# Kernel tuning notes

Hardware: AMD Instinct MI355X
Metric: run time of the kernel (lower is better)

The kernel has to match this reference:

```python
import jax, jax.numpy as jnp
import numpy as np

CHANNELS = 1024
HEADS = 16


def setup_inputs() -> dict:
    key = jax.random.key(0)
    k1, k2, k3, k4 = jax.random.split(key, 4)
    x = jax.random.normal(k1, (32, 8192, CHANNELS), dtype=jnp.float32)
    query = jax.random.normal(k2, (HEADS, CHANNELS), dtype=jnp.float32)
    proj_w = jax.random.normal(k3, (CHANNELS, CHANNELS), dtype=jnp.float32) * (CHANNELS ** -0.5)
    proj_b = jax.random.normal(k4, (CHANNELS,), dtype=jnp.float32) * 0.01
    return {"x": x, "query": query, "proj_w": proj_w, "proj_b": proj_b}


def reference(x, query, proj_w, proj_b):
    scale = x.shape[-1] ** -0.5
    # scores: [b, t, h]
    scores = jnp.einsum('btc,hc->bth', x, query) * scale
    attn = jax.nn.softmax(scores, axis=1)  # softmax over sequence dim
    pooled = jnp.einsum('bth,btc->bhc', attn, x)  # [b, h, c]
    pooled = pooled.mean(axis=1)  # head-mean -> [b, c]
    return pooled @ proj_w.T + proj_b
```

## Files before the change

### kernel.cpp

```cpp
#include <hip/hip_runtime.h>

#define CHANNELS 1024
#define HEADS 16
#define BATCH 32
#define SEQ 8192
#define NCHUNK 16
#define TCHUNK (SEQ / NCHUNK)

#define ACC_FLOATS (BATCH * NCHUNK * HEADS * CHANNELS)
#define L_OFF      ACC_FLOATS
#define L_FLOATS   (BATCH * NCHUNK * HEADS)
#define PM_OFF     (ACC_FLOATS + L_FLOATS)

__device__ __forceinline__ float dot4(float4 a, float4 b) {
    float s = a.x * b.x;
    s = fmaf(a.y, b.y, s);
    s = fmaf(a.z, b.z, s);
    s = fmaf(a.w, b.w, s);
    return s;
}

__global__ __launch_bounds__(256, 2)
void k1_scores_acc(const float* __restrict__ x, const float* __restrict__ q,
                   float* __restrict__ ws) {
    const int tid  = threadIdx.x;
    const int lane = tid & 63;
    const int w    = tid >> 6;
    const int b    = blockIdx.x >> 4;
    const int ck   = blockIdx.x & 15;

    const int cbase = 4 * lane;

    float4 qr[4][4];
#pragma unroll
    for (int h = 0; h < 4; ++h) {
        const float* qp = q + (4 * w + h) * CHANNELS + cbase;
#pragma unroll
        for (int k = 0; k < 4; ++k)
            qr[h][k] = *(const float4*)(qp + 256 * k);
    }

    float4 acc[4][4];
    float  l[4];
#pragma unroll
    for (int h = 0; h < 4; ++h) {
        l[h] = 0.0f;
#pragma unroll
        for (int k = 0; k < 4; ++k)
            acc[h][k] = make_float4(0.f, 0.f, 0.f, 0.f);
    }

    const float* xrow = x + (size_t)(b * SEQ + ck * TCHUNK) * CHANNELS;
    const float scale = 0.03125f;

    float4 xc[4];
#pragma unroll
    for (int k = 0; k < 4; ++k)
        xc[k] = *(const float4*)(xrow + cbase + 256 * k);

    for (int r = 0; r < TCHUNK; ++r) {
        const int rn = (r + 1 < TCHUNK) ? (r + 1) : r;
        const float* nx = xrow + rn * CHANNELS + cbase;
        float4 xn[4];
#pragma unroll
        for (int k = 0; k < 4; ++k)
            xn[k] = *(const float4*)(nx + 256 * k);

        float p[4];
#pragma unroll
        for (int h = 0; h < 4; ++h) {
            float s = dot4(xc[0], qr[h][0]);
            s += dot4(xc[1], qr[h][1]);
            s += dot4(xc[2], qr[h][2]);
            s += dot4(xc[3], qr[h][3]);
            p[h] = s;
        }

#pragma unroll
        for (int h = 0; h < 4; ++h) {
            p[h] += __shfl_xor(p[h], 32, 64);
            p[h] += __shfl_xor(p[h], 16, 64);
            p[h] += __shfl_xor(p[h],  8, 64);
            p[h] += __shfl_xor(p[h],  4, 64);
            p[h] += __shfl_xor(p[h],  2, 64);
            p[h] += __shfl_xor(p[h],  1, 64);
        }

#pragma unroll
        for (int h = 0; h < 4; ++h) {
            const float e = __expf(p[h] * scale);
            l[h] += e;
#pragma unroll
            for (int k = 0; k < 4; ++k) {
                acc[h][k].x = fmaf(e, xc[k].x, acc[h][k].x);
                acc[h][k].y = fmaf(e, xc[k].y, acc[h][k].y);
                acc[h][k].z = fmaf(e, xc[k].z, acc[h][k].z);
                acc[h][k].w = fmaf(e, xc[k].w, acc[h][k].w);
            }
        }

#pragma unroll
        for (int k = 0; k < 4; ++k) xc[k] = xn[k];
    }

    const int blk = b * NCHUNK + ck;
    float* accp = ws + ((size_t)(blk * HEADS + 4 * w)) * CHANNELS;
#pragma unroll
    for (int h = 0; h < 4; ++h) {
#pragma unroll
        for (int k = 0; k < 4; ++k)
            *(float4*)(accp + h * CHANNELS + cbase + 256 * k) = acc[h][k];
    }
    if (lane == 0) {
        *(float4*)(ws + L_OFF + blk * HEADS + 4 * w) =
            make_float4(l[0], l[1], l[2], l[3]);
    }
}

__global__ __launch_bounds__(256)
void k2_merge(float* __restrict__ ws) {
    const int b = blockIdx.x;
    const int tid = threadIdx.x;

    __shared__ float lt[HEADS][NCHUNK + 1];
    __shared__ float linv[HEADS];

    {
        const int h = tid & 15, ck = tid >> 4;
        lt[h][ck] = ws[L_OFF + (b * NCHUNK + ck) * HEADS + h];
    }
    __syncthreads();
    if (tid < HEADS) {
        float s = 0.f;
#pragma unroll
        for (int ck = 0; ck < NCHUNK; ++ck) s += lt[tid][ck];
        linv[tid] = 1.0f / (16.0f * s);
    }
    __syncthreads();

    const int c = 4 * tid;
    float4 pm = make_float4(0.f, 0.f, 0.f, 0.f);
#pragma unroll 1
    for (int h = 0; h < HEADS; ++h) {
        float4 hs = make_float4(0.f, 0.f, 0.f, 0.f);
        for (int ck = 0; ck < NCHUNK; ++ck) {
            const float4 v =
                *(const float4*)(ws + ((size_t)((b * NCHUNK + ck) * HEADS + h)) * CHANNELS + c);
            hs.x += v.x; hs.y += v.y; hs.z += v.z; hs.w += v.w;
        }
        const float wi = linv[h];
        pm.x = fmaf(wi, hs.x, pm.x);
        pm.y = fmaf(wi, hs.y, pm.y);
        pm.z = fmaf(wi, hs.z, pm.z);
        pm.w = fmaf(wi, hs.w, pm.w);
    }
    *(float4*)(ws + PM_OFF + b * CHANNELS + c) = pm;
}

__global__ __launch_bounds__(64)
void k3_proj(const float* __restrict__ W, const float* __restrict__ bias,
             const float* __restrict__ ws, float* __restrict__ out) {
    const int lane = threadIdx.x;
    const int b  = blockIdx.x >> 4;
    const int jt = blockIdx.x & 15;
    const int cbase = 4 * lane;

    const float* pm = ws + PM_OFF + b * CHANNELS;
    float4 pmr[4];
#pragma unroll
    for (int k = 0; k < 4; ++k)
        pmr[k] = *(const float4*)(pm + cbase + 256 * k);

    for (int jj = 0; jj < 64; ++jj) {
        const int j = jt * 64 + jj;
        const float* wr = W + (size_t)j * CHANNELS + cbase;
        float s = 0.f;
#pragma unroll
        for (int k = 0; k < 4; ++k)
            s += dot4(*(const float4*)(wr + 256 * k), pmr[k]);

        s += __shfl_xor(s, 32, 64);
        s += __shfl_xor(s, 16, 64);
        s += __shfl_xor(s,  8, 64);
        s += __shfl_xor(s,  4, 64);
        s += __shfl_xor(s,  2, 64);
        s += __shfl_xor(s,  1, 64);

        if (lane == 0) out[b * CHANNELS + j] = s + bias[j];
    }
}

extern "C" void kernel_launch(void* const* d_in, const int* in_sizes, int n_in,
                              void* d_out, int out_size, void* d_ws, size_t ws_size,
                              hipStream_t stream) {
    const float* x    = (const float*)d_in[0];
    const float* q    = (const float*)d_in[1];
    const float* W    = (const float*)d_in[2];
    const float* bias = (const float*)d_in[3];
    float* out = (float*)d_out;
    float* ws  = (float*)d_ws;

    k1_scores_acc<<<dim3(BATCH * NCHUNK), dim3(256), 0, stream>>>(x, q, ws);
    k2_merge<<<dim3(BATCH), dim3(256), 0, stream>>>(ws);
    k3_proj<<<dim3(BATCH * 16), dim3(64), 0, stream>>>(W, bias, ws, out);
}
```

Baseline: 1.545 ms.

## Transpose-reduce head scores, unroll row loop by two, widen merge and proj grids

The score reduction in k1 now exchanges partial sums across lane halves so that 4 heads share one butterfly: three select-and-shuffle steps plus four full shuffles instead of 24. Each lane then computes one exp2 and redistributes the values with shuffles, and the output head index is remapped to match. The row loop is unrolled by two with ping-pong prefetch buffers. k2 is split across 8 column tiles per batch with a shared-memory reduction over chunks, and k3 uses twice as many blocks, to raise parallelism in the small tail kernels. The main aim is to cut shuffle and ALU overhead in the dominant k1 loop, which may already be bound by memory bandwidth.

Result: faster. 1.503 ms (-2.7%).

```diff
diff --git a/kernel.cpp b/kernel.cpp
--- a/kernel.cpp
+++ b/kernel.cpp
@@ -19,6 +19,8 @@
     s = fmaf(a.w, b.w, s);
     return s;
 }
+
+#define SCALE2 0.045084690834743236f
 
 __global__ __launch_bounds__(256, 2)
 void k1_scores_acc(const float* __restrict__ x, const float* __restrict__ q,
@@ -29,7 +31,10 @@
     const int b    = blockIdx.x >> 4;
     const int ck   = blockIdx.x & 15;
 
-    const int cbase = 4 * lane;
+    const int  cbase = 4 * lane;
+    const bool hi32  = (lane & 32) != 0;
+    const bool hi16  = (lane & 16) != 0;
+    const int  g     = (lane >> 4) & 3;
 
     float4 qr[4][4];
 #pragma unroll
@@ -43,73 +48,93 @@
     float4 acc[4][4];
     float  l[4];
 #pragma unroll
-    for (int h = 0; h < 4; ++h) {
-        l[h] = 0.0f;
-#pragma unroll
-        for (int k = 0; k < 4; ++k)
-            acc[h][k] = make_float4(0.f, 0.f, 0.f, 0.f);
-    }
-
-    const float* xrow = x + (size_t)(b * SEQ + ck * TCHUNK) * CHANNELS;
-    const float scale = 0.03125f;
-
-    float4 xc[4];
+    for (int j = 0; j < 4; ++j) {
+        l[j] = 0.0f;
+#pragma unroll
+        for (int k = 0; k < 4; ++k)
+            acc[j][k] = make_float4(0.f, 0.f, 0.f, 0.f);
+    }
+
+    const float* xrow = x + (size_t)(b * SEQ + ck * TCHUNK) * CHANNELS + cbase;
+
+#define PROCESS_ROW(XC)                                                        \
+    {                                                                          \
+        float p0 = dot4(XC[0], qr[0][0]); p0 += dot4(XC[1], qr[0][1]);         \
+        p0 += dot4(XC[2], qr[0][2]);      p0 += dot4(XC[3], qr[0][3]);         \
+        float p1 = dot4(XC[0], qr[1][0]); p1 += dot4(XC[1], qr[1][1]);         \
+        p1 += dot4(XC[2], qr[1][2]);      p1 += dot4(XC[3], qr[1][3]);         \
+        float p2 = dot4(XC[0], qr[2][0]); p2 += dot4(XC[1], qr[2][1]);         \
+        p2 += dot4(XC[2], qr[2][2]);      p2 += dot4(XC[3], qr[2][3]);         \
+        float p3 = dot4(XC[0], qr[3][0]); p3 += dot4(XC[1], qr[3][1]);         \
+        p3 += dot4(XC[2], qr[3][2]);      p3 += dot4(XC[3], qr[3][3]);         \
+                                       \
+        float tA = hi32 ? p0 : p2;                                             \
+        float rA = __shfl_xor(tA, 32, 64);                                     \
+        float A  = (hi32 ? p2 : p0) + rA;                    \
+        float tB = hi32 ? p1 : p3;                                             \
+        float rB = __shfl_xor(tB, 32, 64);                                     \
+        float B  = (hi32 ? p3 : p1) + rB;                    \
+                                       \
+        float tC = hi16 ? A : B;                                               \
+        float rC = __shfl_xor(tC, 16, 64);                                     \
+        float S  = (hi16 ? B : A) + rC;                            \
+                                          \
+        S += __shfl_xor(S, 8, 64);                                             \
+        S += __shfl_xor(S, 4, 64);                                             \
+        S += __shfl_xor(S, 2, 64);                                             \
+        S += __shfl_xor(S, 1, 64);                                             \
+                    \
+        const float E0 = exp2f(S * SCALE2);                      \
+        const float E1 = __shfl_xor(E0, 16, 64);                 \
+        const float E2 = __shfl_xor(E0, 32, 64);                 \
+        const float E3 = __shfl_xor(E1, 32, 64);                 \
+        const float e[4] = {E0, E1, E2, E3};                                   \
+        l[0] += E0; l[1] += E1; l[2] += E2; l[3] += E3;                        \
+        _Pragma("unroll")                                                      \
+        for (int j = 0; j < 4; ++j) {                                          \
+            const float ev = e[j];                                             \
+            _Pragma("unroll")                                                  \
+            for (int k = 0; k < 4; ++k) {                                      \
+                acc[j][k].x = fmaf(ev, XC[k].x, acc[j][k].x);                  \
+                acc[j][k].y = fmaf(ev, XC[k].y, acc[j][k].y);                  \
+                acc[j][k].z = fmaf(ev, XC[k].z, acc[j][k].z);                  \
+                acc[j][k].w = fmaf(ev, XC[k].w, acc[j][k].w);                  \
+            }                                                                  \
+        }                                                                      \
+    }
+
+    float4 xa[4], xb[4];
 #pragma unroll
     for (int k = 0; k < 4; ++k)
-        xc[k] = *(const float4*)(xrow + cbase + 256 * k);
-
-    for (int r = 0; r < TCHUNK; ++r) {
-        const int rn = (r + 1 < TCHUNK) ? (r + 1) : r;
-        const float* nx = xrow + rn * CHANNELS + cbase;
-        float4 xn[4];
-#pragma unroll
-        for (int k = 0; k < 4; ++k)
-            xn[k] = *(const float4*)(nx + 256 * k);
-
-        float p[4];
-#pragma unroll
-        for (int h = 0; h < 4; ++h) {
-            float s = dot4(xc[0], qr[h][0]);
-            s += dot4(xc[1], qr[h][1]);
-            s += dot4(xc[2], qr[h][2]);
-            s += dot4(xc[3], qr[h][3]);
-            p[h] = s;
-        }
-
-#pragma unroll
-        for (int h = 0; h < 4; ++h) {
-            p[h] += __shfl_xor(p[h], 32, 64);
-            p[h] += __shfl_xor(p[h], 16, 64);
-            p[h] += __shfl_xor(p[h],  8, 64);
-            p[h] += __shfl_xor(p[h],  4, 64);
-            p[h] += __shfl_xor(p[h],  2, 64);
-            p[h] += __shfl_xor(p[h],  1, 64);
-        }
-
-#pragma unroll
-        for (int h = 0; h < 4; ++h) {
-            const float e = __expf(p[h] * scale);
-            l[h] += e;
-#pragma unroll
-            for (int k = 0; k < 4; ++k) {
-                acc[h][k].x = fmaf(e, xc[k].x, acc[h][k].x);
-                acc[h][k].y = fmaf(e, xc[k].y, acc[h][k].y);
-                acc[h][k].z = fmaf(e, xc[k].z, acc[h][k].z);
-                acc[h][k].w = fmaf(e, xc[k].w, acc[h][k].w);
-            }
-        }
-
-#pragma unroll
-        for (int k = 0; k < 4; ++k) xc[k] = xn[k];
-    }
+        xa[k] = *(const float4*)(xrow + 256 * k);
+
+    for (int r = 0; r < TCHUNK; r += 2) {
+        {
+            const float* nx = xrow + (size_t)(r + 1) * CHANNELS;
+#pragma unroll
+            for (int k = 0; k < 4; ++k)
+                xb[k] = *(const float4*)(nx + 256 * k);
+        }
+        PROCESS_ROW(xa)
+        {
+            const int rn = (r + 2 < TCHUNK) ? (r + 2) : (TCHUNK - 1);
+            const float* nx = xrow + (size_t)rn * CHANNELS;
+#pragma unroll
+            for (int k = 0; k < 4; ++k)
+                xa[k] = *(const float4*)(nx + 256 * k);
+        }
+        PROCESS_ROW(xb)
+    }
+#undef PROCESS_ROW
 
     const int blk = b * NCHUNK + ck;
     float* accp = ws + ((size_t)(blk * HEADS + 4 * w)) * CHANNELS;
 #pragma unroll
-    for (int h = 0; h < 4; ++h) {
-#pragma unroll
-        for (int k = 0; k < 4; ++k)
-            *(float4*)(accp + h * CHANNELS + cbase + 256 * k) = acc[h][k];
+    for (int j = 0; j < 4; ++j) {
+        const int h = g ^ j;
+#pragma unroll
+        for (int k = 0; k < 4; ++k)
+            *(float4*)(accp + h * CHANNELS + cbase + 256 * k) = acc[j][k];
     }
     if (lane == 0) {
         *(float4*)(ws + L_OFF + blk * HEADS + 4 * w) =
@@ -119,11 +144,13 @@
 
 __global__ __launch_bounds__(256)
 void k2_merge(float* __restrict__ ws) {
-    const int b = blockIdx.x;
-    const int tid = threadIdx.x;
-
-    __shared__ float lt[HEADS][NCHUNK + 1];
-    __shared__ float linv[HEADS];
+    const int b    = blockIdx.x >> 3;
+    const int tile = blockIdx.x & 7;
+    const int tid  = threadIdx.x;
+
+    __shared__ float  lt[HEADS][NCHUNK];
+    __shared__ float  linv[HEADS];
+    __shared__ float4 red[8][32];
 
     {
         const int h = tid & 15, ck = tid >> 4;
@@ -138,12 +165,17 @@
     }
     __syncthreads();
 
-    const int c = 4 * tid;
+    const int col = tid & 31;
+    const int sub = tid >> 5;
+    const int c   = tile * 128 + col * 4;
+
     float4 pm = make_float4(0.f, 0.f, 0.f, 0.f);
 #pragma unroll 1
     for (int h = 0; h < HEADS; ++h) {
         float4 hs = make_float4(0.f, 0.f, 0.f, 0.f);
-        for (int ck = 0; ck < NCHUNK; ++ck) {
+#pragma unroll
+        for (int d = 0; d < 2; ++d) {
+            const int ck = 2 * sub + d;
             const float4 v =
                 *(const float4*)(ws + ((size_t)((b * NCHUNK + ck) * HEADS + h)) * CHANNELS + c);
             hs.x += v.x; hs.y += v.y; hs.z += v.z; hs.w += v.w;
@@ -154,15 +186,25 @@
         pm.z = fmaf(wi, hs.z, pm.z);
         pm.w = fmaf(wi, hs.w, pm.w);
     }
-    *(float4*)(ws + PM_OFF + b * CHANNELS + c) = pm;
+    red[sub][col] = pm;
+    __syncthreads();
+    if (tid < 32) {
+        float4 s = red[0][tid];
+#pragma unroll
+        for (int u = 1; u < 8; ++u) {
+            const float4 v = red[u][tid];
+            s.x += v.x; s.y += v.y; s.z += v.z; s.w += v.w;
+        }
+        *(float4*)(ws + PM_OFF + b * CHANNELS + tile * 128 + tid * 4) = s;
+    }
 }
 
 __global__ __launch_bounds__(64)
 void k3_proj(const float* __restrict__ W, const float* __restrict__ bias,
              const float* __restrict__ ws, float* __restrict__ out) {
     const int lane = threadIdx.x;
-    const int b  = blockIdx.x >> 4;
-    const int jt = blockIdx.x & 15;
+    const int b  = blockIdx.x >> 5;
+    const int jt = blockIdx.x & 31;
     const int cbase = 4 * lane;
 
     const float* pm = ws + PM_OFF + b * CHANNELS;
@@ -171,8 +213,9 @@
     for (int k = 0; k < 4; ++k)
         pmr[k] = *(const float4*)(pm + cbase + 256 * k);
 
-    for (int jj = 0; jj < 64; ++jj) {
-        const int j = jt * 64 + jj;
+#pragma unroll 2
+    for (int jj = 0; jj < 32; ++jj) {
+        const int j = jt * 32 + jj;
         const float* wr = W + (size_t)j * CHANNELS + cbase;
         float s = 0.f;
 #pragma unroll
@@ -201,6 +244,6 @@
     float* ws  = (float*)d_ws;
 
     k1_scores_acc<<<dim3(BATCH * NCHUNK), dim3(256), 0, stream>>>(x, q, ws);
-    k2_merge<<<dim3(BATCH), dim3(256), 0, stream>>>(ws);
-    k3_proj<<<dim3(BATCH * 16), dim3(64), 0, stream>>>(W, bias, ws, out);
-}
+    k2_merge<<<dim3(BATCH * 8), dim3(256), 0, stream>>>(ws);
+    k3_proj<<<dim3(BATCH * 32), dim3(64), 0, stream>>>(W, bias, ws, out);
+}
```
